# Optimization experiments

Measured on AMD Instinct MI355X. Metric: run time of the kernel, lower is better.

## Reference

```python
import math
import jax, jax.numpy as jnp
import numpy as np

B, S, D, H = 2, 2048, 1024, 16
HD = D // H  # 64


def setup_inputs() -> dict:
    key = jax.random.key(0)
    k = jax.random.split(key, 8)
    x = jax.random.normal(k[0], (B, S, D), dtype=jnp.float32)
    # RoPE tables: inv_freq over half dim, emb = concat(freqs, freqs)
    inv_freq = 1.0 / (10000.0 ** (jnp.arange(0, HD, 2, dtype=jnp.float32) / HD))
    pos = jnp.arange(S, dtype=jnp.float32)
    freqs = pos[:, None] * inv_freq[None, :]            # [S, HD/2]
    emb = jnp.concatenate([freqs, freqs], axis=-1)      # [S, HD]
    cos = jnp.cos(emb)[:, None, :]                      # [S, 1, HD] broadcasts over [B,S,H,HD]
    sin = jnp.sin(emb)[:, None, :]
    # causal additive mask [1, 1, S, S]
    neg = jnp.finfo(jnp.float32).min
    mask = jnp.where(jnp.tril(jnp.ones((S, S), dtype=bool)), 0.0, neg)[None, None]
    scale = 0.02
    wq = jax.random.normal(k[1], (D, D), dtype=jnp.float32) * scale
    wk = jax.random.normal(k[2], (D, D), dtype=jnp.float32) * scale
    wv = jax.random.normal(k[3], (D, D), dtype=jnp.float32) * scale
    wo = jax.random.normal(k[4], (D, D), dtype=jnp.float32) * scale
    return {"x": x, "cos": cos, "sin": sin, "mask": mask,
            "wq": wq, "wk": wk, "wv": wv, "wo": wo}


def rotate_half(t):
    t1, t2 = t[..., : t.shape[-1] // 2], t[..., t.shape[-1] // 2:]
    return jnp.concatenate([-t2, t1], axis=-1)


def reference(x, cos, sin, mask, wq, wk, wv, wo):
    b, s, d = x.shape
    # torch nn.Linear: y = x @ W^T  (W is [out, in])
    q = (x @ wq.T).reshape(b, s, H, HD)
    kk = (x @ wk.T).reshape(b, s, H, HD)
    v = (x @ wv.T).reshape(b, s, H, HD)
    q = q * cos + rotate_half(q) * sin
    kk = kk * cos + rotate_half(kk) * sin
    q = q.transpose(0, 2, 1, 3)   # [b, h, s, hd]
    kk = kk.transpose(0, 2, 1, 3)
    v = v.transpose(0, 2, 1, 3)
    scores = jnp.einsum('bhqd,bhkd->bhqk', q, kk) / math.sqrt(HD)
    scores = scores + mask
    probs = jax.nn.softmax(scores.astype(jnp.float32), axis=-1).astype(q.dtype)
    out = jnp.einsum('bhqk,bhkd->bhqd', probs, v)
    out = out.transpose(0, 2, 1, 3).reshape(b, s, d)
    return out @ wo.T
```

## Files before the change

kernel.cpp:

```cpp
#include <hip/hip_runtime.h>
#include <hip/hip_bf16.h>

typedef __hip_bfloat16 bf16;
typedef unsigned short u16;
typedef __attribute__((ext_vector_type(8))) short short8;
typedef __attribute__((ext_vector_type(4))) float floatx4;

constexpr int B_ = 2, S_ = 2048, D_ = 1024, H_ = 16, HD_ = 64;
constexpr int QT = 64, KT = 64, PAD = 72;
constexpr int NQT = S_ / QT;
constexpr int GK = 1024, BK = 64;

__device__ inline float b2f(u16 u) {
    union { unsigned int i; float f; } v; v.i = ((unsigned int)u) << 16; return v.f;
}
__device__ inline u16 f2b(float f) {
    bf16 h = __float2bfloat16(f); return *(u16*)&h;
}

__device__ inline void gl16(const u16* g, u16* l) {
    __builtin_amdgcn_global_load_lds(
        (const __attribute__((address_space(1))) unsigned int*)g,
        (__attribute__((address_space(3))) unsigned int*)l, 16, 0, 0);
}

__global__ __launch_bounds__(256) void cvt_kernel(
    const float* __restrict__ x,  const float* __restrict__ wq,
    const float* __restrict__ wk, const float* __restrict__ wv,
    const float* __restrict__ wo,
    u16* __restrict__ Xb, u16* __restrict__ Wb)
{
    const size_t c = (size_t)blockIdx.x * 256 + threadIdx.x;
    const float* src; u16* dst; size_t off;
    if (c < (size_t)(1 << 19)) { src = x; dst = Xb; off = c; }
    else {
        const size_t w = c - (1 << 19);
        const int wi = (int)(w >> 17);
        off = w & ((1 << 17) - 1);
        src = (wi == 0) ? wq : (wi == 1) ? wk : (wi == 2) ? wv : wo;
        dst = Wb + ((size_t)wi << 20);
    }
    const float4 a = *(const float4*)(src + off * 8);
    const float4 b = *(const float4*)(src + off * 8 + 4);
    ushort4 u0; u0.x = f2b(a.x); u0.y = f2b(a.y); u0.z = f2b(a.z); u0.w = f2b(a.w);
    ushort4 u1; u1.x = f2b(b.x); u1.y = f2b(b.y); u1.z = f2b(b.z); u1.w = f2b(b.w);
    *(ushort4*)(dst + off * 8)     = u0;
    *(ushort4*)(dst + off * 8 + 4) = u1;
}

template <typename TC, int SCATTER, int ROPE, int BN>
__global__ __launch_bounds__(256) void gemm_async(
    const u16* __restrict__ A, const u16* __restrict__ Wb,
    const float* __restrict__ cosp, const float* __restrict__ sinp,
    TC* __restrict__ C0, TC* __restrict__ C1, TC* __restrict__ C2, int N)
{
    constexpr int NT = BN / 32;

    int x, y, z;
    {
        const int xcd = blockIdx.x & 7, idx = blockIdx.x >> 3;
        y = (xcd & 3) * 8 + (idx & 7);
        if (BN == 128) {
            const int xz = (xcd >> 2) * 12 + (idx >> 3);
            x = xz & 7; z = xz >> 3;
        } else {
            x = (xcd >> 2) * 8 + (idx >> 3);
            z = 0;
        }
    }

    const u16* W = Wb + ((size_t)z << 20);
    TC*        C = (z == 0) ? C0 : (z == 1 ? C1 : C2);

    __shared__ __align__(16) u16 As[128 * BK];
    __shared__ __align__(16) u16 Bs[BN * BK];

    const int tid  = threadIdx.x;
    const int wave = tid >> 6, lane = tid & 63;
    const int quad = lane >> 4, l16 = lane & 15;
    const int wm = wave >> 1, wn = wave & 1;
    const int m0 = y * 128, n0 = x * BN;

    const int srl = lane >> 3;
    const int sc  = (lane & 7) ^ srl;

    floatx4 acc[4][NT] = {};

    for (int k0 = 0; k0 < GK; k0 += BK) {
        __syncthreads();
#pragma unroll
        for (int j = 0; j < 4; ++j) {
            const int rb = wave * 32 + j * 8;
            gl16(A + (size_t)(m0 + rb + srl) * GK + k0 + sc * 8, &As[rb * BK]);
        }
#pragma unroll
        for (int j = 0; j < BN / 32; ++j) {
            const int rb = wave * (BN / 4) + j * 8;
            gl16(W + (size_t)(n0 + rb + srl) * GK + k0 + sc * 8, &Bs[rb * BK]);
        }
        __syncthreads();

#pragma unroll
        for (int ks = 0; ks < 2; ++ks) {
            short8 af[4], bfr[NT];
#pragma unroll
            for (int mt = 0; mt < 4; ++mt) {
                const int R = wm * 64 + mt * 16 + l16;
                af[mt] = *(const short8*)&As[R * BK + (((ks * 4 + quad) ^ (l16 & 7)) * 8)];
            }
#pragma unroll
            for (int nt = 0; nt < NT; ++nt) {
                const int R = wn * (BN / 2) + nt * 16 + l16;
                bfr[nt] = *(const short8*)&Bs[R * BK + (((ks * 4 + quad) ^ (l16 & 7)) * 8)];
            }
#pragma unroll
            for (int mt = 0; mt < 4; ++mt)
#pragma unroll
                for (int nt = 0; nt < NT; ++nt)
                    acc[mt][nt] = __builtin_amdgcn_mfma_f32_16x16x32_bf16(
                        af[mt], bfr[nt], acc[mt][nt], 0, 0, 0);
        }
    }

    if (ROPE && z < 2) {
        const float scale = (z == 0) ? 0.125f * 1.44269504f : 1.0f;
        const int h = (n0 + wn * 64) >> 6;
#pragma unroll
        for (int mt = 0; mt < 4; ++mt)
#pragma unroll
            for (int r = 0; r < 4; ++r) {
                const int m = m0 + wm * 64 + mt * 16 + quad * 4 + r;
                const int b = m >> 11, s = m & (S_ - 1);
                const size_t base = ((size_t)(b * H_ + h) * S_ + s) << 6;
#pragma unroll
                for (int np = 0; np < 2; ++np) {
                    const int d = np * 16 + l16;
                    const float c1 = cosp[s * HD_ + d];
                    const float s1 = sinp[s * HD_ + d];
                    const float c2 = cosp[s * HD_ + d + 32];
                    const float s2 = sinp[s * HD_ + d + 32];
                    const float q0 = acc[mt][np][r], q1 = acc[mt][np + 2][r];
                    ((bf16*)C)[base + d]      = __float2bfloat16((q0 * c1 - q1 * s1) * scale);
                    ((bf16*)C)[base + d + 32] = __float2bfloat16((q1 * c2 + q0 * s2) * scale);
                }
            }
    } else if (SCATTER) {
        const int h = (n0 + wn * 64) >> 6;
#pragma unroll
        for (int mt = 0; mt < 4; ++mt)
#pragma unroll
            for (int nt = 0; nt < NT; ++nt)
#pragma unroll
                for (int r = 0; r < 4; ++r) {
                    const int m = m0 + wm * 64 + mt * 16 + quad * 4 + r;
                    const int b = m >> 11, s = m & (S_ - 1);
                    const int hd = nt * 16 + l16;
                    ((bf16*)C)[(((size_t)(b * H_ + h) * S_ + s) << 6) + hd] =
                        __float2bfloat16(acc[mt][nt][r]);
                }
    } else {
#pragma unroll
        for (int mt = 0; mt < 4; ++mt)
#pragma unroll
            for (int nt = 0; nt < NT; ++nt)
#pragma unroll
                for (int r = 0; r < 4; ++r) {
                    const int m = m0 + wm * 64 + mt * 16 + quad * 4 + r;
                    const int n = n0 + wn * (BN / 2) + nt * 16 + l16;
                    ((float*)C)[(size_t)m * N + n] = acc[mt][nt][r];
                }
    }
}

__global__ __launch_bounds__(256) void vt_kernel(
    const u16* __restrict__ V, u16* __restrict__ Vt)
{
    __shared__ u16 T[HD_ * 72];
    const int s0 = blockIdx.x * 64;
    const int bh = blockIdx.z * H_ + blockIdx.y;
    const int tid = threadIdx.x;
    const int r = tid >> 2, c = (tid & 3) * 16;

    const u16* src = V + ((size_t)bh * S_ + s0 + r) * HD_ + c;
    const short8 v0 = *(const short8*)src;
    const short8 v1 = *(const short8*)(src + 8);
#pragma unroll
    for (int j = 0; j < 8; ++j) {
        T[(c + j)     * 72 + r] = (u16)v0[j];
        T[(c + 8 + j) * 72 + r] = (u16)v1[j];
    }
    __syncthreads();
    const short8 o0 = *(const short8*)&T[r * 72 + c];
    const short8 o1 = *(const short8*)&T[r * 72 + c + 8];
    u16* dst = Vt + ((size_t)bh * HD_ + r) * S_ + s0 + c;
    *(short8*)dst       = o0;
    *(short8*)(dst + 8) = o1;
}

__global__ __launch_bounds__(256) void fa_kernel(
    const u16* __restrict__ Qg, const u16* __restrict__ Kg, const u16* __restrict__ Vt,
    bf16* __restrict__ Og)
{
    __shared__ __align__(16) u16 Kt[2][KT * PAD];
    __shared__ __align__(16) u16 Vs[2][HD_ * PAD];
    __shared__ __align__(16) u16 Pt[4 * 16 * PAD];

    const int flat = blockIdx.x;
    const int bx = flat >> 5;
    const int bh = flat & 31;
    const int b  = bh >> 4, h = bh & 15;
    const int tid  = threadIdx.x;
    const int wave = tid >> 6, lane = tid & 63;
    const int quad = lane >> 4, l16 = lane & 15;
    const int srow = tid >> 2, scol = (tid & 3) * 16;

    for (int half = 0; half < 2; ++half) {
        const int qt = half ? (NQT - 1 - bx) : bx;
        const int qb = qt * QT;

        const u16* qrow = Qg + ((size_t)bh * S_ + qb + wave * 16 + l16) * HD_;
        const short8 aq0 = *(const short8*)(qrow + quad * 8);
        const short8 aq1 = *(const short8*)(qrow + 32 + quad * 8);

        floatx4 oacc[4] = {{0,0,0,0},{0,0,0,0},{0,0,0,0},{0,0,0,0}};
        float lsum = 0.f;

        __syncthreads();
        {
            const u16* kp = Kg + ((size_t)bh * S_ + srow) * HD_ + scol;
            *(short8*)&Kt[0][srow * PAD + scol]     = *(const short8*)kp;
            *(short8*)&Kt[0][srow * PAD + scol + 8] = *(const short8*)(kp + 8);
            const u16* vp = Vt + ((size_t)bh * HD_ + srow) * S_ + scol;
            *(short8*)&Vs[0][srow * PAD + scol]     = *(const short8*)vp;
            *(short8*)&Vs[0][srow * PAD + scol + 8] = *(const short8*)(vp + 8);
        }
        __syncthreads();

        for (int it = 0; it <= qt; ++it) {
            const int  cur = it & 1;
            const bool pf  = (it < qt);
            short8 nk0, nk1, nv0, nv1;
            if (pf) {
                const int kb = (it + 1) * KT;
                const u16* kp = Kg + ((size_t)bh * S_ + kb + srow) * HD_ + scol;
                nk0 = *(const short8*)kp; nk1 = *(const short8*)(kp + 8);
                const u16* vp = Vt + ((size_t)bh * HD_ + srow) * S_ + kb + scol;
                nv0 = *(const short8*)vp; nv1 = *(const short8*)(vp + 8);
            }

            floatx4 sacc[4] = {{0,0,0,0},{0,0,0,0},{0,0,0,0},{0,0,0,0}};
#pragma unroll
            for (int kt = 0; kt < 4; ++kt) {
                const short8 bk0 = *(const short8*)&Kt[cur][(kt * 16 + l16) * PAD + quad * 8];
                const short8 bk1 = *(const short8*)&Kt[cur][(kt * 16 + l16) * PAD + 32 + quad * 8];
                sacc[kt] = __builtin_amdgcn_mfma_f32_16x16x32_bf16(bk0, aq0, sacc[kt], 0, 0, 0);
                sacc[kt] = __builtin_amdgcn_mfma_f32_16x16x32_bf16(bk1, aq1, sacc[kt], 0, 0, 0);
            }

            if (it == qt) {
                const int ql = wave * 16 + l16;
#pragma unroll
                for (int kt = 0; kt < 4; ++kt)
#pragma unroll
                    for (int r = 0; r < 4; ++r)
                        if (kt * 16 + quad * 4 + r > ql) sacc[kt][r] = -1.0e38f;
            }

            float rs = 0.f;
#pragma unroll
            for (int kt = 0; kt < 4; ++kt) {
                const float e0 = __builtin_amdgcn_exp2f(sacc[kt][0]);
                const float e1 = __builtin_amdgcn_exp2f(sacc[kt][1]);
                const float e2 = __builtin_amdgcn_exp2f(sacc[kt][2]);
                const float e3 = __builtin_amdgcn_exp2f(sacc[kt][3]);
                rs += (e0 + e1) + (e2 + e3);
                ushort4 pk; pk.x = f2b(e0); pk.y = f2b(e1); pk.z = f2b(e2); pk.w = f2b(e3);
                *(ushort4*)&Pt[(wave * 16 + l16) * PAD + kt * 16 + quad * 4] = pk;
            }
            rs += __shfl_xor(rs, 16);
            rs += __shfl_xor(rs, 32);
            lsum += rs;

            const short8 ap0 = *(const short8*)&Pt[(wave * 16 + l16) * PAD + quad * 8];
            const short8 ap1 = *(const short8*)&Pt[(wave * 16 + l16) * PAD + 32 + quad * 8];

#pragma unroll
            for (int dt = 0; dt < 4; ++dt) {
                const short8 bv0 = *(const short8*)&Vs[cur][(dt * 16 + l16) * PAD + quad * 8];
                const short8 bv1 = *(const short8*)&Vs[cur][(dt * 16 + l16) * PAD + 32 + quad * 8];
                oacc[dt] = __builtin_amdgcn_mfma_f32_16x16x32_bf16(bv0, ap0, oacc[dt], 0, 0, 0);
                oacc[dt] = __builtin_amdgcn_mfma_f32_16x16x32_bf16(bv1, ap1, oacc[dt], 0, 0, 0);
            }

            if (pf) {
                const int nb = cur ^ 1;
                *(short8*)&Kt[nb][srow * PAD + scol]     = nk0;
                *(short8*)&Kt[nb][srow * PAD + scol + 8] = nk1;
                *(short8*)&Vs[nb][srow * PAD + scol]     = nv0;
                *(short8*)&Vs[nb][srow * PAD + scol + 8] = nv1;
            }
            __syncthreads();
        }

        const float inv = 1.0f / lsum;
        bf16* orow = Og + ((size_t)(b * S_ + qb + wave * 16 + l16)) * D_ + h * HD_;
#pragma unroll
        for (int dt = 0; dt < 4; ++dt) {
            ushort4 pk;
            pk.x = f2b(oacc[dt][0] * inv);
            pk.y = f2b(oacc[dt][1] * inv);
            pk.z = f2b(oacc[dt][2] * inv);
            pk.w = f2b(oacc[dt][3] * inv);
            *(ushort4*)((u16*)orow + dt * 16 + quad * 4) = pk;
        }
    }
}

extern "C" void kernel_launch(void* const* d_in, const int* in_sizes, int n_in,
                              void* d_out, int out_size, void* d_ws, size_t ws_size,
                              hipStream_t stream)
{
    const float* x    = (const float*)d_in[0];
    const float* cosp = (const float*)d_in[1];
    const float* sinp = (const float*)d_in[2];
    const float* wq   = (const float*)d_in[4];
    const float* wk   = (const float*)d_in[5];
    const float* wv   = (const float*)d_in[6];
    const float* wo   = (const float*)d_in[7];
    float* out = (float*)d_out;

    u16* w0 = (u16*)d_ws;
    const size_t NE = (size_t)B_ * S_ * D_;
    u16* Qb  = w0;
    u16* Kb  = w0 + NE;
    u16* Vb  = w0 + 2 * NE;
    u16* Vtb = w0 + 3 * NE;
    u16* Xb  = w0 + 4 * NE;
    u16* Wb  = w0 + 5 * NE;
    u16* Ab  = Xb;
    u16* Wob = Wb + 3 * (1 << 20);

    cvt_kernel<<<4096, 256, 0, stream>>>(x, wq, wk, wv, wo, Xb, Wb);

    gemm_async<bf16, 1, 1, 128><<<768, 256, 0, stream>>>(
        Xb, Wb, cosp, sinp, (bf16*)Qb, (bf16*)Kb, (bf16*)Vb, D_);

    vt_kernel<<<dim3(S_ / 64, H_, B_), 256, 0, stream>>>(Vb, Vtb);

    fa_kernel<<<dim3((NQT / 2) * 32, 1, 1), 256, 0, stream>>>(Qb, Kb, Vtb, (bf16*)Ab);

    gemm_async<float, 0, 0, 64><<<512, 256, 0, stream>>>(
        Ab, Wob, cosp, sinp, out, out, out, D_);
}
```

Measured before the change: 201.5 us.

## Fuse V transpose into QKV GEMM epilogue and stage RoPE tables in LDS

The QKV projection GEMM now writes V directly in transposed [b,h,hd,s] layout with packed 4-element bf16 stores, so the separate vt_kernel launch and its extra round trip through global memory are removed. The RoPE epilogue first loads a tile of cos/sin (first 32 columns only, since the table repeats across its two halves) into the shared memory already used for the A/B tiles, then reads from LDS instead of doing four scattered global loads per element. This adds two barriers to the epilogue and depends on the cos/sin halves being identical, which holds for the standard RoPE construction.

Measured after the change: 197.6 us. Within noise of the previous version (-1.9%).

```diff
diff --git a/kernel.cpp b/kernel.cpp
--- a/kernel.cpp
+++ b/kernel.cpp
@@ -123,41 +123,57 @@
     }
 
     if (ROPE && z < 2) {
+        float* Cs = (float*)As;
+        float* Sn = (float*)Bs;
+        const int s0 = m0 & (S_ - 1);
+        const int bq = m0 >> 11;
+        __syncthreads();
+        {
+            const int rr = tid >> 1;
+            const int cc = (tid & 1) * 16;
+            const float4* cp = (const float4*)(cosp + (size_t)(s0 + rr) * HD_ + cc);
+            const float4* sp = (const float4*)(sinp + (size_t)(s0 + rr) * HD_ + cc);
+            float4* cd = (float4*)&Cs[rr * 32 + cc];
+            float4* sd = (float4*)&Sn[rr * 32 + cc];
+            cd[0] = cp[0]; cd[1] = cp[1]; cd[2] = cp[2]; cd[3] = cp[3];
+            sd[0] = sp[0]; sd[1] = sp[1]; sd[2] = sp[2]; sd[3] = sp[3];
+        }
+        __syncthreads();
+
         const float scale = (z == 0) ? 0.125f * 1.44269504f : 1.0f;
-        const int h = (n0 + wn * 64) >> 6;
+        const int h = (n0 >> 6) + wn;
 #pragma unroll
         for (int mt = 0; mt < 4; ++mt)
 #pragma unroll
             for (int r = 0; r < 4; ++r) {
-                const int m = m0 + wm * 64 + mt * 16 + quad * 4 + r;
-                const int b = m >> 11, s = m & (S_ - 1);
-                const size_t base = ((size_t)(b * H_ + h) * S_ + s) << 6;
+                const int mr = wm * 64 + mt * 16 + quad * 4 + r;
+                const size_t base = ((size_t)(bq * H_ + h) * S_ + s0 + mr) << 6;
 #pragma unroll
                 for (int np = 0; np < 2; ++np) {
                     const int d = np * 16 + l16;
-                    const float c1 = cosp[s * HD_ + d];
-                    const float s1 = sinp[s * HD_ + d];
-                    const float c2 = cosp[s * HD_ + d + 32];
-                    const float s2 = sinp[s * HD_ + d + 32];
+                    const float c1 = Cs[mr * 32 + d];
+                    const float s1 = Sn[mr * 32 + d];
                     const float q0 = acc[mt][np][r], q1 = acc[mt][np + 2][r];
                     ((bf16*)C)[base + d]      = __float2bfloat16((q0 * c1 - q1 * s1) * scale);
-                    ((bf16*)C)[base + d + 32] = __float2bfloat16((q1 * c2 + q0 * s2) * scale);
+                    ((bf16*)C)[base + d + 32] = __float2bfloat16((q1 * c1 + q0 * s1) * scale);
                 }
             }
     } else if (SCATTER) {
-        const int h = (n0 + wn * 64) >> 6;
+        const int s0 = m0 & (S_ - 1);
+        const int bq = m0 >> 11;
+        const int h  = (n0 >> 6) + wn;
+        const int bh = bq * H_ + h;
 #pragma unroll
         for (int mt = 0; mt < 4; ++mt)
 #pragma unroll
-            for (int nt = 0; nt < NT; ++nt)
-#pragma unroll
-                for (int r = 0; r < 4; ++r) {
-                    const int m = m0 + wm * 64 + mt * 16 + quad * 4 + r;
-                    const int b = m >> 11, s = m & (S_ - 1);
-                    const int hd = nt * 16 + l16;
-                    ((bf16*)C)[(((size_t)(b * H_ + h) * S_ + s) << 6) + hd] =
-                        __float2bfloat16(acc[mt][nt][r]);
-                }
+            for (int nt = 0; nt < NT; ++nt) {
+                const int hd = nt * 16 + l16;
+                const int sb = s0 + wm * 64 + mt * 16 + quad * 4;
+                ushort4 pk;
+                pk.x = f2b(acc[mt][nt][0]); pk.y = f2b(acc[mt][nt][1]);
+                pk.z = f2b(acc[mt][nt][2]); pk.w = f2b(acc[mt][nt][3]);
+                *(ushort4*)&((u16*)C)[((size_t)(bh * HD_ + hd) << 11) + sb] = pk;
+            }
     } else {
 #pragma unroll
         for (int mt = 0; mt < 4; ++mt)
@@ -170,31 +186,6 @@
                     ((float*)C)[(size_t)m * N + n] = acc[mt][nt][r];
                 }
     }
-}
-
-__global__ __launch_bounds__(256) void vt_kernel(
-    const u16* __restrict__ V, u16* __restrict__ Vt)
-{
-    __shared__ u16 T[HD_ * 72];
-    const int s0 = blockIdx.x * 64;
-    const int bh = blockIdx.z * H_ + blockIdx.y;
-    const int tid = threadIdx.x;
-    const int r = tid >> 2, c = (tid & 3) * 16;
-
-    const u16* src = V + ((size_t)bh * S_ + s0 + r) * HD_ + c;
-    const short8 v0 = *(const short8*)src;
-    const short8 v1 = *(const short8*)(src + 8);
-#pragma unroll
-    for (int j = 0; j < 8; ++j) {
-        T[(c + j)     * 72 + r] = (u16)v0[j];
-        T[(c + 8 + j) * 72 + r] = (u16)v1[j];
-    }
-    __syncthreads();
-    const short8 o0 = *(const short8*)&T[r * 72 + c];
-    const short8 o1 = *(const short8*)&T[r * 72 + c + 8];
-    u16* dst = Vt + ((size_t)bh * HD_ + r) * S_ + s0 + c;
-    *(short8*)dst       = o0;
-    *(short8*)(dst + 8) = o1;
 }
 
 __global__ __launch_bounds__(256) void fa_kernel(
@@ -333,19 +324,16 @@
     const size_t NE = (size_t)B_ * S_ * D_;
     u16* Qb  = w0;
     u16* Kb  = w0 + NE;
-    u16* Vb  = w0 + 2 * NE;
-    u16* Vtb = w0 + 3 * NE;
-    u16* Xb  = w0 + 4 * NE;
-    u16* Wb  = w0 + 5 * NE;
+    u16* Vtb = w0 + 2 * NE;
+    u16* Xb  = w0 + 3 * NE;
+    u16* Wb  = w0 + 4 * NE;
     u16* Ab  = Xb;
     u16* Wob = Wb + 3 * (1 << 20);
 
     cvt_kernel<<<4096, 256, 0, stream>>>(x, wq, wk, wv, wo, Xb, Wb);
 
     gemm_async<bf16, 1, 1, 128><<<768, 256, 0, stream>>>(
-        Xb, Wb, cosp, sinp, (bf16*)Qb, (bf16*)Kb, (bf16*)Vb, D_);
-
-    vt_kernel<<<dim3(S_ / 64, H_, B_), 256, 0, stream>>>(Vb, Vtb);
+        Xb, Wb, cosp, sinp, (bf16*)Qb, (bf16*)Kb, (bf16*)Vtb, D_);
 
     fa_kernel<<<dim3((NQT / 2) * 32, 1, 1), 256, 0, stream>>>(Qb, Kb, Vtb, (bf16*)Ab);
 
```
